# Performance work log

Hardware: AMD Instinct MI355X
Metric: run time of the kernel (lower is better)

## Reference

```python
import jax, jax.numpy as jnp
import numpy as np

N_NODES = 10000
N_EDGES = 160000
F_IN, D, DEPTH, F_OUT = 6, 512, 10, 1


def setup_inputs() -> dict:
    key = jax.random.key(0)
    ks = jax.random.split(key, 10)
    features = jax.random.normal(ks[0], (N_NODES, F_IN), dtype=jnp.float32)
    src = jax.random.randint(ks[1], (N_EDGES,), 0, N_NODES, dtype=jnp.int32)
    dst = jax.random.randint(ks[2], (N_EDGES,), 0, N_NODES, dtype=jnp.int32)
    s_in = 1.0 / np.sqrt(F_IN)
    s_h = 1.0 / np.sqrt(D)
    W_in = jax.random.uniform(ks[3], (F_IN, D), jnp.float32, -s_in, s_in)
    b_in = jax.random.uniform(ks[4], (D,), jnp.float32, -s_in, s_in)
    Ws = jax.random.uniform(ks[5], (DEPTH, D, D), jnp.float32, -s_h, s_h)
    bs = jax.random.uniform(ks[6], (DEPTH, D), jnp.float32, -s_h, s_h)
    W_out = jax.random.uniform(ks[7], (D, F_OUT), jnp.float32, -s_h, s_h)
    b_out = jax.random.uniform(ks[8], (F_OUT,), jnp.float32, -s_h, s_h)
    return {"features": features, "W_in": W_in, "b_in": b_in, "Ws": Ws,
            "bs": bs, "W_out": W_out, "b_out": b_out, "src": src, "dst": dst}


def reference(features, W_in, b_in, Ws, bs, W_out, b_out, src, dst):
    n = features.shape[0]
    # GCNLayer: aggregate = scatter-sum of neighbor features (copy_src + sum), then Linear
    agg = jax.ops.segment_sum(features[src], dst, num_segments=n)  # [N, F_in]
    x = jax.nn.relu(agg @ W_in + b_in)  # ReLU only after input layer (per forward)

    def step(x, wb):
        W, b = wb
        a = jax.ops.segment_sum(x[src], dst, num_segments=n)  # [N, D]
        return a @ W + b, None  # no activation between hidden GCN layers

    x, _ = jax.lax.scan(step, x, (Ws, bs))
    return x @ W_out + b_out  # [N, 1]
```

## Files before the change

### kernel.cpp

```cpp
#include <hip/hip_runtime.h>


#define N_NODES 10000
#define N_EDGES 160000
#define DEPTH   10

#define NB      80
#define BT      512
#define NTH     (NB * BT)
#define NPB     125
#define ECAP    4096

__device__ __forceinline__ float ldA(const float* p) {
    return __hip_atomic_load(p, __ATOMIC_RELAXED, __HIP_MEMORY_SCOPE_AGENT);
}
__device__ __forceinline__ int ldAi(const int* p) {
    return __hip_atomic_load(p, __ATOMIC_RELAXED, __HIP_MEMORY_SCOPE_AGENT);
}
__device__ __forceinline__ void stA(float* p, float v) {
    __hip_atomic_store(p, v, __ATOMIC_RELAXED, __HIP_MEMORY_SCOPE_AGENT);
}
__device__ __forceinline__ void stAi(int* p, int v) {
    __hip_atomic_store(p, v, __ATOMIC_RELAXED, __HIP_MEMORY_SCOPE_AGENT);
}

__device__ __forceinline__ void gbar(int* arrive, int phase) {
    const int tx = threadIdx.x;
    const int bx = blockIdx.x;
    const int target = phase + 1;
    asm volatile("s_waitcnt vmcnt(0)" ::: "memory");
    __syncthreads();
    if (tx == 0) stAi(&arrive[bx * 32], target);
    if (tx < NB && tx != bx) {
        while (ldAi(&arrive[tx * 32]) < target) __builtin_amdgcn_s_sleep(1);
    }
    __syncthreads();
}

__device__ __forceinline__ void chain_step(int s, int gw, int lane,
                                           const float* __restrict__ Ws,
                                           const float* __restrict__ bs,
                                           const float* __restrict__ W_out,
                                           float* __restrict__ vbufs,
                                           float* __restrict__ gamma) {
    const int w = gw - 8;
    if (w < 0 || w > 512) return;
    const int l = 9 - s;
    float vin[8];
    if (s == 0) {
#pragma unroll
        for (int c = 0; c < 8; c++) vin[c] = W_out[lane + 64 * c];
    } else {
        const float* vb = vbufs + (s & 1) * 512;
#pragma unroll
        for (int c = 0; c < 8; c++) vin[c] = ldA(vb + lane + 64 * c);
    }
    float acc = 0.f;
    if (w < 512) {
        const float* Wr = Ws + (size_t)l * (512 * 512) + (size_t)w * 512;
#pragma unroll
        for (int c = 0; c < 8; c++) acc += Wr[lane + 64 * c] * vin[c];
    } else {
        const float* bl = bs + (size_t)l * 512;
#pragma unroll
        for (int c = 0; c < 8; c++) acc += bl[lane + 64 * c] * vin[c];
    }
#pragma unroll
    for (int off = 32; off; off >>= 1) acc += __shfl_xor(acc, off, 64);
    if (lane == 0) {
        if (w < 512) stA(vbufs + ((s + 1) & 1) * 512 + w, acc);
        else         stA(gamma + l, acc);
    }
}

extern "C" __global__ void __launch_bounds__(BT, 1) gcn_mega(
    const float* __restrict__ features, const float* __restrict__ W_in,
    const float* __restrict__ b_in, const float* __restrict__ Ws,
    const float* __restrict__ bs, const float* __restrict__ W_out,
    const float* __restrict__ b_out, const int* __restrict__ src,
    const int* __restrict__ dst, float* __restrict__ out,
    int* arrive, int* deg, int* row_ptr, int* cursor,
    int* esrc, float* vbufs, float* gamma, float* rb0, float* rb1)
{
    __shared__ int   lds_e[ECAP];
    __shared__ float s_Wb[4096];
    __shared__ float s_vt[512];
    __shared__ float s_gam[16];
    __shared__ int   s_info[2];
    __shared__ int   sums[BT];

    const int tx   = threadIdx.x;
    const int bx   = blockIdx.x;
    const int t    = bx * BT + tx;
    const int gw   = t >> 6;
    const int lane = t & 63;
    int bp = 0;

    for (int e = t; e < N_EDGES; e += NTH) atomicAdd(&deg[dst[e]], 1);
    for (int idx = tx; idx < 4096; idx += BT) {
        int j = idx >> 3, k = idx & 7;
        float v = 0.f;
        if (k < 6) v = W_in[k * 512 + j];
        else if (k == 6) v = b_in[j];
        s_Wb[idx] = v;
    }
    chain_step(0, gw, lane, Ws, bs, W_out, vbufs, gamma);
    gbar(arrive, bp); bp++;

    if (bx == 0) {
        const int base = tx * 20;
        const bool sact = base < N_NODES;
        int lv[20];
        int ssum = 0;
        if (sact) {
#pragma unroll
            for (int i = 0; i < 20; i++) { lv[i] = ldAi(&deg[base + i]); ssum += lv[i]; }
        }
        sums[tx] = ssum;
        __syncthreads();
        for (int off = 1; off < BT; off <<= 1) {
            int v = (tx >= off) ? sums[tx - off] : 0;
            __syncthreads();
            sums[tx] += v;
            __syncthreads();
        }
        if (sact) {
            int run = tx ? sums[tx - 1] : 0;
#pragma unroll
            for (int i = 0; i < 20; i++) {
                stAi(&row_ptr[base + i], run);
                stAi(&cursor[base + i], run);
                run += lv[i];
            }
            if (tx == 499) stAi(&row_ptr[N_NODES], run);
        }
    }
    chain_step(1, gw, lane, Ws, bs, W_out, vbufs, gamma);
    gbar(arrive, bp); bp++;

    for (int e = t; e < N_EDGES; e += NTH) {
        int d = dst[e];
        int sv = src[e];
        int pos = atomicAdd(&cursor[d], 1);
        stAi(&esrc[pos], sv);
    }
    chain_step(2, gw, lane, Ws, bs, W_out, vbufs, gamma);
    gbar(arrive, bp); bp++;

    if (tx == 0) {
        s_info[0] = ldAi(&row_ptr[bx * NPB]);
        s_info[1] = ldAi(&row_ptr[bx * NPB + NPB]);
    }
    __syncthreads();
    const int e_lo = s_info[0];
    const int slen = s_info[1] - e_lo;
    const bool use_lds = (slen <= ECAP);
    if (use_lds) {
        for (int i = tx; i < slen; i += BT) lds_e[i] = ldAi(&esrc[e_lo + i]);
    }
    __syncthreads();

    const int node = bx * NPB + (tx >> 2);
    const int sub  = tx & 3;
    const bool act = tx < 4 * NPB;
    int ns = 0, ne = 0;
    float a0 = 0.f, a1 = 0.f, a2 = 0.f, a3 = 0.f, a4 = 0.f, a5 = 0.f;
    if (act) {
        ns = ldAi(&row_ptr[node]);
        ne = ldAi(&row_ptr[node + 1]);
        if (use_lds) {
            for (int pp = ns + sub; pp < ne; pp += 4) {
                int j = lds_e[pp - e_lo];
                const float2* f = (const float2*)(features + (size_t)j * 6);
                float2 f0 = f[0], f1 = f[1], f2 = f[2];
                a0 += f0.x; a1 += f0.y; a2 += f1.x;
                a3 += f1.y; a4 += f2.x; a5 += f2.y;
            }
        } else {
            for (int pp = ns + sub; pp < ne; pp += 4) {
                int j = ldAi(&esrc[pp]);
                const float2* f = (const float2*)(features + (size_t)j * 6);
                float2 f0 = f[0], f1 = f[1], f2 = f[2];
                a0 += f0.x; a1 += f0.y; a2 += f1.x;
                a3 += f1.y; a4 += f2.x; a5 += f2.y;
            }
        }
        a0 += __shfl_xor(a0, 1, 64); a0 += __shfl_xor(a0, 2, 64);
        a1 += __shfl_xor(a1, 1, 64); a1 += __shfl_xor(a1, 2, 64);
        a2 += __shfl_xor(a2, 1, 64); a2 += __shfl_xor(a2, 2, 64);
        a3 += __shfl_xor(a3, 1, 64); a3 += __shfl_xor(a3, 2, 64);
        a4 += __shfl_xor(a4, 1, 64); a4 += __shfl_xor(a4, 2, 64);
        a5 += __shfl_xor(a5, 1, 64); a5 += __shfl_xor(a5, 2, 64);
    }
    chain_step(3, gw, lane, Ws, bs, W_out, vbufs, gamma);
    gbar(arrive, bp); bp++;

    for (int s = 4; s <= 9; s++) {
        chain_step(s, gw, lane, Ws, bs, W_out, vbufs, gamma);
        gbar(arrive, bp); bp++;
    }

    s_vt[tx & 511] = ldA(&vbufs[tx & 511]);
    if (tx < DEPTH) s_gam[tx] = ldA(&gamma[tx]);
    __syncthreads();
    if (act) {
        const float4* Wb4 = (const float4*)s_Wb;
        float zacc = 0.f;
#pragma unroll 4
        for (int jj = 0; jj < 128; jj++) {
            int j = (jj << 2) | sub;
            float4 wA = Wb4[2 * j];
            float4 wB = Wb4[2 * j + 1];
            float tv = wB.z + a0 * wA.x + a1 * wA.y + a2 * wA.z +
                       a3 * wA.w + a4 * wB.x + a5 * wB.y;
            zacc += fmaxf(tv, 0.f) * s_vt[j];
        }
        zacc += __shfl_xor(zacc, 1, 64);
        zacc += __shfl_xor(zacc, 2, 64);
        if (sub == 0) stA(&rb0[node], zacc);
    }
    gbar(arrive, bp); bp++;

    for (int l = 0; l < DEPTH; l++) {
        if (act) {
            const float* rin = (l & 1) ? rb1 : rb0;
            float h0 = 0.f, h1 = 0.f;
            int pp = ns + sub;
            if (use_lds) {
                for (; pp + 4 < ne; pp += 8) {
                    h0 += ldA(&rin[lds_e[pp - e_lo]]);
                    h1 += ldA(&rin[lds_e[pp + 4 - e_lo]]);
                }
                if (pp < ne) h0 += ldA(&rin[lds_e[pp - e_lo]]);
            } else {
                for (; pp + 4 < ne; pp += 8) {
                    h0 += ldA(&rin[ldAi(&esrc[pp])]);
                    h1 += ldA(&rin[ldAi(&esrc[pp + 4])]);
                }
                if (pp < ne) h0 += ldA(&rin[ldAi(&esrc[pp])]);
            }
            float hs = h0 + h1;
            hs += __shfl_xor(hs, 1, 64);
            hs += __shfl_xor(hs, 2, 64);
            if (sub == 0) {
                float res = hs + s_gam[l];
                if (l == DEPTH - 1) out[node] = res + b_out[0];
                else stA(&((l & 1) ? rb0 : rb1)[node], res);
            }
        }
        if (l < DEPTH - 1) { gbar(arrive, bp); bp++; }
    }
}


extern "C" void kernel_launch(void* const* d_in, const int* in_sizes, int n_in,
                              void* d_out, int out_size, void* d_ws, size_t ws_size,
                              hipStream_t stream) {
    const float* features = (const float*)d_in[0];
    const float* W_in     = (const float*)d_in[1];
    const float* b_in     = (const float*)d_in[2];
    const float* Ws       = (const float*)d_in[3];
    const float* bs       = (const float*)d_in[4];
    const float* W_out    = (const float*)d_in[5];
    const float* b_out    = (const float*)d_in[6];
    const int*   src      = (const int*)d_in[7];
    const int*   dst      = (const int*)d_in[8];
    float* out = (float*)d_out;

    char* base = (char*)d_ws;
    int*   arrive  = (int*)(base + 0);
    int*   deg     = (int*)(base + 10240);
    int*   row_ptr = (int*)(base + 50432);
    int*   cursor  = (int*)(base + 90624);
    int*   esrc    = (int*)(base + 130688);
    float* vbufs   = (float*)(base + 770688);
    float* gamma   = (float*)(base + 774784);
    float* rb0     = (float*)(base + 774912);
    float* rb1     = (float*)(base + 814976);

    hipMemsetAsync(base, 0, 50240, stream);

    gcn_mega<<<NB, BT, 0, stream>>>(features, W_in, b_in, Ws, bs, W_out, b_out,
                                    src, dst, out,
                                    arrive, deg, row_ptr, cursor,
                                    esrc, vbufs, gamma, rb0, rb1);
}
```

Measured before the change: 195.4 us.

## Split persistent kernel into separate graph and weight-chain block groups

Blocks are split into two groups. 40 blocks of 1024 threads do the graph work: CSR build, input aggregation and the propagation layers. 33 blocks compute the back-propagated weight chain (W_out through Ws) using their own group barrier, and the graph group waits on a one-time rendezvous flag before it needs that result. Each group's barriers now involve fewer blocks, and the chain's 10 dependent steps overlap the CSR build instead of being interleaved into every global barrier. The block-level prefix scan is also rewritten with wave shuffles. The risk is that the graph phase now runs on only 40 blocks with 250 nodes each.

```diff
diff --git a/kernel.cpp b/kernel.cpp
--- a/kernel.cpp
+++ b/kernel.cpp
@@ -5,11 +5,13 @@
 #define N_EDGES 160000
 #define DEPTH   10
 
-#define NB      80
-#define BT      512
-#define NTH     (NB * BT)
-#define NPB     125
-#define ECAP    4096
+#define NB_G 40
+#define NB_C 33
+#define NB   (NB_G + NB_C)
+#define BT   1024
+#define NTHG (NB_G * BT)
+#define NPB  250
+#define ECAP 8192
 
 __device__ __forceinline__ float ldA(const float* p) {
     return __hip_atomic_load(p, __ATOMIC_RELAXED, __HIP_MEMORY_SCOPE_AGENT);
@@ -24,53 +26,15 @@
     __hip_atomic_store(p, v, __ATOMIC_RELAXED, __HIP_MEMORY_SCOPE_AGENT);
 }
 
-__device__ __forceinline__ void gbar(int* arrive, int phase) {
+__device__ __forceinline__ void group_bar(int* flags, int gi, int n, int target) {
     const int tx = threadIdx.x;
-    const int bx = blockIdx.x;
-    const int target = phase + 1;
     asm volatile("s_waitcnt vmcnt(0)" ::: "memory");
     __syncthreads();
-    if (tx == 0) stAi(&arrive[bx * 32], target);
-    if (tx < NB && tx != bx) {
-        while (ldAi(&arrive[tx * 32]) < target) __builtin_amdgcn_s_sleep(1);
-    }
-    __syncthreads();
-}
-
-__device__ __forceinline__ void chain_step(int s, int gw, int lane,
-                                           const float* __restrict__ Ws,
-                                           const float* __restrict__ bs,
-                                           const float* __restrict__ W_out,
-                                           float* __restrict__ vbufs,
-                                           float* __restrict__ gamma) {
-    const int w = gw - 8;
-    if (w < 0 || w > 512) return;
-    const int l = 9 - s;
-    float vin[8];
-    if (s == 0) {
-#pragma unroll
-        for (int c = 0; c < 8; c++) vin[c] = W_out[lane + 64 * c];
-    } else {
-        const float* vb = vbufs + (s & 1) * 512;
-#pragma unroll
-        for (int c = 0; c < 8; c++) vin[c] = ldA(vb + lane + 64 * c);
-    }
-    float acc = 0.f;
-    if (w < 512) {
-        const float* Wr = Ws + (size_t)l * (512 * 512) + (size_t)w * 512;
-#pragma unroll
-        for (int c = 0; c < 8; c++) acc += Wr[lane + 64 * c] * vin[c];
-    } else {
-        const float* bl = bs + (size_t)l * 512;
-#pragma unroll
-        for (int c = 0; c < 8; c++) acc += bl[lane + 64 * c] * vin[c];
-    }
-#pragma unroll
-    for (int off = 32; off; off >>= 1) acc += __shfl_xor(acc, off, 64);
-    if (lane == 0) {
-        if (w < 512) stA(vbufs + ((s + 1) & 1) * 512 + w, acc);
-        else         stA(gamma + l, acc);
-    }
+    if (tx == 0) stAi(&flags[gi * 32], target);
+    if (tx < n && tx != gi) {
+        while (ldAi(&flags[tx * 32]) < target) __builtin_amdgcn_s_sleep(1);
+    }
+    __syncthreads();
 }
 
 extern "C" __global__ void __launch_bounds__(BT, 1) gcn_mega(
@@ -79,24 +43,64 @@
     const float* __restrict__ bs, const float* __restrict__ W_out,
     const float* __restrict__ b_out, const int* __restrict__ src,
     const int* __restrict__ dst, float* __restrict__ out,
-    int* arrive, int* deg, int* row_ptr, int* cursor,
-    int* esrc, float* vbufs, float* gamma, float* rb0, float* rb1)
+    int* g_arrive, int* c_arrive, int* rdv, int* deg, int* row_ptr,
+    int* cursor, int* esrc, float* vbufs, float* gamma,
+    float* rb0, float* rb1)
 {
     __shared__ int   lds_e[ECAP];
     __shared__ float s_Wb[4096];
     __shared__ float s_vt[512];
     __shared__ float s_gam[16];
     __shared__ int   s_info[2];
-    __shared__ int   sums[BT];
-
-    const int tx   = threadIdx.x;
-    const int bx   = blockIdx.x;
-    const int t    = bx * BT + tx;
-    const int gw   = t >> 6;
-    const int lane = t & 63;
-    int bp = 0;
-
-    for (int e = t; e < N_EDGES; e += NTH) atomicAdd(&deg[dst[e]], 1);
+    __shared__ int   s_wsum[16];
+
+    const int tx = threadIdx.x;
+    const int bx = blockIdx.x;
+
+    if (bx >= NB_G) {
+        const int gi   = bx - NB_G;
+        const int cw   = gi * (BT / 64) + (tx >> 6);
+        const int lane = tx & 63;
+        for (int s = 0; s < DEPTH; s++) {
+            const int l = 9 - s;
+            if (cw <= 512) {
+                float vin[8];
+                if (s == 0) {
+#pragma unroll
+                    for (int c = 0; c < 8; c++) vin[c] = W_out[lane + 64 * c];
+                } else {
+                    const float* vb = vbufs + (s & 1) * 512;
+#pragma unroll
+                    for (int c = 0; c < 8; c++) vin[c] = ldA(vb + lane + 64 * c);
+                }
+                const float* rowp = (cw < 512)
+                    ? (Ws + (size_t)l * (512 * 512) + (size_t)cw * 512)
+                    : (bs + (size_t)l * 512);
+                float acc = 0.f;
+#pragma unroll
+                for (int c = 0; c < 8; c++) acc += rowp[lane + 64 * c] * vin[c];
+#pragma unroll
+                for (int off = 32; off; off >>= 1) acc += __shfl_xor(acc, off, 64);
+                if (lane == 0) {
+                    if (cw < 512) stA(&vbufs[((s + 1) & 1) * 512 + cw], acc);
+                    else          stA(&gamma[l], acc);
+                }
+            }
+            if (s < DEPTH - 1) group_bar(c_arrive, gi, NB_C, s + 1);
+        }
+        asm volatile("s_waitcnt vmcnt(0)" ::: "memory");
+        __syncthreads();
+        if (tx == 0) stAi(&rdv[gi * 32], 1);
+        return;
+    }
+
+    const int gi = bx;
+    int gt = 1;
+
+    {
+        const int t0 = bx * BT + tx;
+        for (int e = t0; e < N_EDGES; e += NTHG) atomicAdd(&deg[dst[e]], 1);
+    }
     for (int idx = tx; idx < 4096; idx += BT) {
         int j = idx >> 3, k = idx & 7;
         float v = 0.f;
@@ -104,48 +108,58 @@
         else if (k == 6) v = b_in[j];
         s_Wb[idx] = v;
     }
-    chain_step(0, gw, lane, Ws, bs, W_out, vbufs, gamma);
-    gbar(arrive, bp); bp++;
+    group_bar(g_arrive, gi, NB_G, gt++);
 
     if (bx == 0) {
-        const int base = tx * 20;
-        const bool sact = base < N_NODES;
-        int lv[20];
+        const int lane = tx & 63, wid = tx >> 6;
+        const bool sact = tx < 1000;
+        int lv[10];
         int ssum = 0;
         if (sact) {
 #pragma unroll
-            for (int i = 0; i < 20; i++) { lv[i] = ldAi(&deg[base + i]); ssum += lv[i]; }
-        }
-        sums[tx] = ssum;
+            for (int i = 0; i < 10; i++) { lv[i] = ldAi(&deg[tx * 10 + i]); ssum += lv[i]; }
+        }
+        int v = ssum;
+#pragma unroll
+        for (int off = 1; off < 64; off <<= 1) {
+            int u = __shfl_up(v, off, 64);
+            if (lane >= off) v += u;
+        }
+        if (lane == 63) s_wsum[wid] = v;
         __syncthreads();
-        for (int off = 1; off < BT; off <<= 1) {
-            int v = (tx >= off) ? sums[tx - off] : 0;
-            __syncthreads();
-            sums[tx] += v;
-            __syncthreads();
-        }
+        if (wid == 0) {
+            int w = (lane < 16) ? s_wsum[lane] : 0;
+#pragma unroll
+            for (int off = 1; off < 16; off <<= 1) {
+                int u = __shfl_up(w, off, 64);
+                if (lane >= off) w += u;
+            }
+            if (lane < 16) s_wsum[lane] = w;
+        }
+        __syncthreads();
         if (sact) {
-            int run = tx ? sums[tx - 1] : 0;
-#pragma unroll
-            for (int i = 0; i < 20; i++) {
-                stAi(&row_ptr[base + i], run);
-                stAi(&cursor[base + i], run);
+            int run = (wid ? s_wsum[wid - 1] : 0) + (v - ssum);
+#pragma unroll
+            for (int i = 0; i < 10; i++) {
+                stAi(&row_ptr[tx * 10 + i], run);
+                stAi(&cursor[tx * 10 + i], run);
                 run += lv[i];
             }
-            if (tx == 499) stAi(&row_ptr[N_NODES], run);
-        }
-    }
-    chain_step(1, gw, lane, Ws, bs, W_out, vbufs, gamma);
-    gbar(arrive, bp); bp++;
-
-    for (int e = t; e < N_EDGES; e += NTH) {
-        int d = dst[e];
-        int sv = src[e];
-        int pos = atomicAdd(&cursor[d], 1);
-        stAi(&esrc[pos], sv);
-    }
-    chain_step(2, gw, lane, Ws, bs, W_out, vbufs, gamma);
-    gbar(arrive, bp); bp++;
+            if (tx == 999) stAi(&row_ptr[N_NODES], run);
+        }
+    }
+    group_bar(g_arrive, gi, NB_G, gt++);
+
+    {
+        const int t0 = bx * BT + tx;
+        for (int e = t0; e < N_EDGES; e += NTHG) {
+            int d = dst[e];
+            int sv = src[e];
+            int pos = atomicAdd(&cursor[d], 1);
+            stAi(&esrc[pos], sv);
+        }
+    }
+    group_bar(g_arrive, gi, NB_G, gt++);
 
     if (tx == 0) {
         s_info[0] = ldAi(&row_ptr[bx * NPB]);
@@ -192,17 +206,15 @@
         a4 += __shfl_xor(a4, 1, 64); a4 += __shfl_xor(a4, 2, 64);
         a5 += __shfl_xor(a5, 1, 64); a5 += __shfl_xor(a5, 2, 64);
     }
-    chain_step(3, gw, lane, Ws, bs, W_out, vbufs, gamma);
-    gbar(arrive, bp); bp++;
-
-    for (int s = 4; s <= 9; s++) {
-        chain_step(s, gw, lane, Ws, bs, W_out, vbufs, gamma);
-        gbar(arrive, bp); bp++;
-    }
-
-    s_vt[tx & 511] = ldA(&vbufs[tx & 511]);
-    if (tx < DEPTH) s_gam[tx] = ldA(&gamma[tx]);
-    __syncthreads();
+
+    if (tx < NB_C) {
+        while (ldAi(&rdv[tx * 32]) < 1) __builtin_amdgcn_s_sleep(1);
+    }
+    __syncthreads();
+    if (tx < 512) s_vt[tx] = ldA(&vbufs[tx]);
+    if (tx >= 512 && tx < 512 + DEPTH) s_gam[tx - 512] = ldA(&gamma[tx - 512]);
+    __syncthreads();
+
     if (act) {
         const float4* Wb4 = (const float4*)s_Wb;
         float zacc = 0.f;
@@ -219,7 +231,7 @@
         zacc += __shfl_xor(zacc, 2, 64);
         if (sub == 0) stA(&rb0[node], zacc);
     }
-    gbar(arrive, bp); bp++;
+    group_bar(g_arrive, gi, NB_G, gt++);
 
     for (int l = 0; l < DEPTH; l++) {
         if (act) {
@@ -248,7 +260,7 @@
                 else stA(&((l & 1) ? rb0 : rb1)[node], res);
             }
         }
-        if (l < DEPTH - 1) { gbar(arrive, bp); bp++; }
+        if (l < DEPTH - 1) group_bar(g_arrive, gi, NB_G, gt++);
     }
 }
 
@@ -268,20 +280,22 @@
     float* out = (float*)d_out;
 
     char* base = (char*)d_ws;
-    int*   arrive  = (int*)(base + 0);
-    int*   deg     = (int*)(base + 10240);
-    int*   row_ptr = (int*)(base + 50432);
-    int*   cursor  = (int*)(base + 90624);
-    int*   esrc    = (int*)(base + 130688);
-    float* vbufs   = (float*)(base + 770688);
-    float* gamma   = (float*)(base + 774784);
-    float* rb0     = (float*)(base + 774912);
-    float* rb1     = (float*)(base + 814976);
-
-    hipMemsetAsync(base, 0, 50240, stream);
+    int*   g_arrive = (int*)(base + 0);
+    int*   c_arrive = (int*)(base + 5120);
+    int*   rdv      = (int*)(base + 10240);
+    int*   deg      = (int*)(base + 15360);
+    int*   row_ptr  = (int*)(base + 55424);
+    int*   cursor   = (int*)(base + 95488);
+    int*   esrc     = (int*)(base + 135552);
+    float* vbufs    = (float*)(base + 775552);
+    float* gamma    = (float*)(base + 779648);
+    float* rb0      = (float*)(base + 779712);
+    float* rb1      = (float*)(base + 819712);
+
+    hipMemsetAsync(base, 0, 55360, stream);
 
     gcn_mega<<<NB, BT, 0, stream>>>(features, W_in, b_in, Ws, bs, W_out, b_out,
                                     src, dst, out,
-                                    arrive, deg, row_ptr, cursor,
-                                    esrc, vbufs, gamma, rb0, rb1);
-}
+                                    g_arrive, c_arrive, rdv, deg, row_ptr,
+                                    cursor, esrc, vbufs, gamma, rb0, rb1);
+}
```

Result: faster. 184.0 us, median of 2 (-5.8%).
